# Kernel tuning notes

Measured on AMD Instinct MI355X. Metric: run time of the kernel, lower is better.

The kernel has to match this reference:

```python
import jax, jax.numpy as jnp
import numpy as np

B, T, D = 32, 1024, 256
TOP_K = 2
EPS_ADJ = 1e-6
LN_EPS = 1e-5


def setup_inputs() -> dict:
    key = jax.random.key(0)
    ks = jax.random.split(key, 10)
    inp = {
        'x': jax.random.normal(ks[0], (B, T, D), dtype=jnp.float32),
        'mask': jnp.ones((B, T), dtype=jnp.int32),
    }
    # two GCN layers: linear W [D_out, D_in] (torch layout), bias, LayerNorm gamma/beta
    for li in range(2):
        inp[f'W{li}'] = jax.random.normal(ks[1 + 4 * li], (D, D), dtype=jnp.float32) * (1.0 / np.sqrt(D))
        inp[f'b{li}'] = jax.random.normal(ks[2 + 4 * li], (D,), dtype=jnp.float32) * 0.02
        inp[f'g{li}'] = jnp.ones((D,), dtype=jnp.float32)
        inp[f'be{li}'] = jnp.zeros((D,), dtype=jnp.float32)
    return inp


def _layer_norm(x, gamma, beta):
    mu = jnp.mean(x, axis=-1, keepdims=True)
    var = jnp.mean(jnp.square(x - mu), axis=-1, keepdims=True)
    return (x - mu) * jax.lax.rsqrt(var + LN_EPS) * gamma + beta


def _cos_sim(x, maskf):
    x_norm = x / jnp.clip(jnp.linalg.norm(x, axis=-1, keepdims=True), 1e-12)
    sim = jnp.einsum('bid,bjd->bij', x_norm, x_norm)
    return sim * (maskf[:, :, None] * maskf[:, None, :])


def _build_adj(sim, maskf):
    b, t, _ = sim.shape
    eye = jnp.eye(t, dtype=sim.dtype)
    # temporal chain edges + self loops
    base_adj = eye + jnp.eye(t, k=1, dtype=sim.dtype) + jnp.eye(t, k=-1, dtype=sim.dtype)
    # top-k over similarity with diagonal suppressed
    corel = jnp.where(eye[None] == 1, -1.0, sim)
    _, topk_inds = jax.lax.top_k(corel, TOP_K)  # [B, T, K]
    bi = jnp.arange(b)[:, None, None]
    ii = jnp.arange(t)[None, :, None]
    ext = jnp.zeros_like(sim).at[bi, ii, topk_inds].set(1.0)
    ext = jnp.maximum(ext, jnp.swapaxes(ext, 1, 2))
    ext = ext * (maskf[:, :, None] * maskf[:, None, :])
    adj = jnp.clip(base_adj[None] + ext, 0.0, 1.0) * sim + eye[None]
    row_sum = jnp.sum(adj, axis=-1, keepdims=True) + EPS_ADJ
    col_sum = jnp.sum(adj, axis=1, keepdims=True) + EPS_ADJ
    adj = adj / jnp.sqrt(row_sum * col_sum)
    return adj * (maskf[:, :, None] * maskf[:, None, :])


def reference(x, mask, W0, b0, g0, be0, W1, b1, g1, be1):
    maskf = mask.astype(x.dtype)
    sim = _cos_sim(x, maskf)
    adj = _build_adj(sim, maskf)
    params = [(W0, b0, g0, be0), (W1, b1, g1, be1)]
    h = x
    for (W, bb, g, be) in params:
        h = jnp.einsum('bij,bjd->bid', adj, h)
        h = jnp.einsum('bid,od->bio', h, W) + bb
        h = jax.nn.elu(h)
        h = _layer_norm(h, g, be)
        # dropout: identity in eval mode
    return h
```

## Files before the change

kernel.cpp:

```cpp
#include <hip/hip_runtime.h>
#include <math.h>

#define NB 32
#define NT 1024
#define ND 256
#define NROWS (NB*NT)
#define MAXE 64

typedef __attribute__((ext_vector_type(8))) short bf16x8;
typedef __attribute__((ext_vector_type(4))) float f32x4;
typedef unsigned short ushort_t;
typedef unsigned long long u64;

__device__ inline ushort_t f2bf_rn(float f){
  unsigned u = __float_as_uint(f);
  unsigned r = u + 0x7fffu + ((u >> 16) & 1u);
  return (ushort_t)(r >> 16);
}
__device__ inline float bf2f(ushort_t h){
  return __uint_as_float(((unsigned)h) << 16);
}
__device__ inline void ceswap(u64 &a, u64 &b){
  u64 mx = a > b ? a : b;
  u64 mn = a > b ? b : a;
  a = mx; b = mn;
}
__device__ inline u64 umax64(u64 a, u64 b){ return a > b ? a : b; }

__device__ inline void gld16(const ushort_t* g, ushort_t* l){
  __builtin_amdgcn_global_load_lds(
      (const __attribute__((address_space(1))) unsigned int*)(g),
      (__attribute__((address_space(3))) unsigned int*)(l),
      16, 0, 0);
}

__global__ __launch_bounds__(256) void k_norm(const float* __restrict__ x,
                                              float* __restrict__ xn,
                                              ushort_t* __restrict__ xh,
                                              ushort_t* __restrict__ xl){
  int row = blockIdx.x;
  int t = threadIdx.x;
  size_t base = (size_t)row*ND;
  float v = x[base + t];
  float ss = v*v;
  #pragma unroll
  for (int off=32; off; off>>=1) ss += __shfl_xor(ss, off);
  __shared__ float sred[4];
  if ((t & 63) == 0) sred[t>>6] = ss;
  __syncthreads();
  float tot = sred[0] + sred[1] + sred[2] + sred[3];
  float nrm = fmaxf(sqrtf(tot), 1e-12f);
  float res = v / nrm;
  xn[base + t] = res;
  ushort_t hb = f2bf_rn(res);
  float lres = res - bf2f(hb);
  xh[base + t] = hb;
  xl[base + t] = f2bf_rn(lres);
}

__global__ __launch_bounds__(256) void k_wsplit(const float* __restrict__ W0,
                                                const float* __restrict__ W1,
                                                ushort_t* __restrict__ Wh0, ushort_t* __restrict__ Wl0,
                                                ushort_t* __restrict__ Wh1, ushort_t* __restrict__ Wl1){
  int idx = blockIdx.x*256 + threadIdx.x;
  float w0 = W0[idx]; ushort_t h0 = f2bf_rn(w0);
  Wh0[idx] = h0; Wl0[idx] = f2bf_rn(w0 - bf2f(h0));
  float w1 = W1[idx]; ushort_t h1 = f2bf_rn(w1);
  Wh1[idx] = h1; Wl1[idx] = f2bf_rn(w1 - bf2f(h1));
}

__global__ __launch_bounds__(256) void k_sim(const ushort_t* __restrict__ xh,
                                             const ushort_t* __restrict__ xl,
                                             ushort_t* __restrict__ S,
                                             int bat0){
  __shared__ __align__(16) ushort_t Ahs[128*64];
  __shared__ __align__(16) ushort_t Als[128*64];
  __shared__ __align__(16) ushort_t Bhs[128*64];
  __shared__ __align__(16) ushort_t Bls[128*64];

  int blk0 = blockIdx.x;
  int blk = (blk0 & 7)*128 + (blk0 >> 3);

  int b_local = blk >> 6;
  int b = bat0 + b_local;
  int tt = blk & 63;
  int ti = tt >> 3, tj = tt & 7;
  int i0 = ti*128, j0 = tj*128;

  int t = threadIdx.x;
  int lane = t & 63, wave = t >> 6;
  int wy = wave >> 1, wx = wave & 1;
  int c = lane & 15, q = lane >> 4;
  int lrow = lane >> 3;
  int sc   = (lane & 7) ^ lrow;

  f32x4 acc[4][4];
  #pragma unroll
  for (int bi=0;bi<4;bi++)
    #pragma unroll
    for (int bj=0;bj<4;bj++) acc[bi][bj] = {0.f,0.f,0.f,0.f};

  size_t rowbA = (size_t)(b*NT + i0);
  size_t rowbB = (size_t)(b*NT + j0);
  const ushort_t* Agh = xh + rowbA*ND;
  const ushort_t* Agl = xl + rowbA*ND;
  const ushort_t* Bgh = xh + rowbB*ND;
  const ushort_t* Bgl = xl + rowbB*ND;

  for (int kc=0; kc<4; kc++){
    __syncthreads();
    int koff = kc*64;
    #pragma unroll
    for (int inst=0; inst<4; inst++){
      int r0 = wave*32 + inst*8;
      size_t go = (size_t)(r0 + lrow)*ND + koff + sc*8;
      gld16(Agh + go, &Ahs[r0*64]);
      gld16(Agl + go, &Als[r0*64]);
      gld16(Bgh + go, &Bhs[r0*64]);
      gld16(Bgl + go, &Bls[r0*64]);
    }
    __syncthreads();

    #pragma unroll
    for (int ks=0; ks<2; ks++){
      bf16x8 ah[4], al[4], bh[4], bl[4];
      int slot = (ks*4 + q) ^ (c & 7);
      #pragma unroll
      for (int bi=0;bi<4;bi++){
        int row = wy*64 + bi*16 + c;
        ah[bi] = *(const bf16x8*)&Ahs[row*64 + slot*8];
        al[bi] = *(const bf16x8*)&Als[row*64 + slot*8];
      }
      #pragma unroll
      for (int bj=0;bj<4;bj++){
        int row = wx*64 + bj*16 + c;
        bh[bj] = *(const bf16x8*)&Bhs[row*64 + slot*8];
        bl[bj] = *(const bf16x8*)&Bls[row*64 + slot*8];
      }
      #pragma unroll
      for (int bi=0;bi<4;bi++)
        #pragma unroll
        for (int bj=0;bj<4;bj++){
          acc[bi][bj] = __builtin_amdgcn_mfma_f32_16x16x32_bf16(ah[bi], bh[bj], acc[bi][bj], 0, 0, 0);
          acc[bi][bj] = __builtin_amdgcn_mfma_f32_16x16x32_bf16(al[bi], bh[bj], acc[bi][bj], 0, 0, 0);
          acc[bi][bj] = __builtin_amdgcn_mfma_f32_16x16x32_bf16(ah[bi], bl[bj], acc[bi][bj], 0, 0, 0);
        }
    }
  }

  size_t srow0 = (size_t)b_local*NT + i0 + wy*64;
  int col0 = j0 + wx*64;
  #pragma unroll
  for (int bi=0;bi<4;bi++){
    #pragma unroll
    for (int reg=0;reg<4;reg++){
      ushort_t* dst = S + (srow0 + bi*16 + q*4 + reg)*NT + col0;
      #pragma unroll
      for (int bj=0;bj<4;bj++)
        dst[bj*16 + c] = f2bf_rn(acc[bi][bj][reg]);
    }
  }
}

__global__ __launch_bounds__(256) void k_top8(const ushort_t* __restrict__ S,
                                              int4* __restrict__ cand4,
                                              int rowbase){
  int row = blockIdx.x*4 + (threadIdx.x >> 6);
  int lane = threadIdx.x & 63;
  int i = row & 1023;
  const ushort_t* Sr = S + (size_t)row*NT;
  u64 e0 = 0, e1 = 0;
  #pragma unroll
  for (int seg=0; seg<4; seg++){
    int col = seg*256 + lane*4;
    u64 v4 = *(const u64*)&Sr[col];
    #pragma unroll
    for (int m=0;m<4;m++){
      unsigned u = (unsigned)((v4 >> (16*m)) & 0xffffu) << 16;
      unsigned key = u ^ ((unsigned)((int)u >> 31) | 0x80000000u);
      int j = col + m;
      u64 e = ((u64)key << 32) | (unsigned)j;
      if (j == i) e = 0;
      u64 mn = e0 > e ? e : e0;
      e0 = e0 > e ? e0 : e;
      e1 = e1 > mn ? e1 : mn;
    }
  }
  u64 L0 = e0, L1 = e1, L2 = 0, L3 = 0;
  #pragma unroll
  for (int st=1; st<64; st<<=1){
    u64 R0 = __shfl_xor(L0, st), R1 = __shfl_xor(L1, st);
    u64 R2 = __shfl_xor(L2, st), R3 = __shfl_xor(L3, st);
    u64 m0 = umax64(L0, R3), m1 = umax64(L1, R2);
    u64 m2 = umax64(L2, R1), m3 = umax64(L3, R0);
    ceswap(m0, m2); ceswap(m1, m3); ceswap(m0, m1); ceswap(m2, m3);
    L0 = m0; L1 = m1; L2 = m2; L3 = m3;
  }
  if (lane == 0)
    cand4[rowbase + row] = make_int4((int)(unsigned)L0, (int)(unsigned)L1,
                                     (int)(unsigned)L2, (int)(unsigned)L3);
}

__global__ __launch_bounds__(64) void k_refine4(const float* __restrict__ xn,
                                                const int4* __restrict__ cand4,
                                                int2* __restrict__ top2){
  int row = blockIdx.x; int b = row >> 10, i = row & 1023;
  int l = threadIdx.x;
  const float* Xb = xn + (size_t)b*NT*ND;
  float4 xi = *(const float4*)&Xb[(size_t)i*ND + l*4];
  int4 cd = cand4[row];
  int cands[4] = {cd.x, cd.y, cd.z, cd.w};
  double bv1=-1e30, bv2=-1e30; int bi1=0x7fffffff, bi2=0x7fffffff;
  #pragma unroll
  for (int cq=0;cq<4;cq++){
    int j = cands[cq];
    float4 xj = *(const float4*)&Xb[(size_t)j*ND + l*4];
    double p = (double)xi.x*xj.x + (double)xi.y*xj.y
             + (double)xi.z*xj.z + (double)xi.w*xj.w;
    #pragma unroll
    for (int off=32; off; off>>=1) p += __shfl_xor(p, off);
    if (p > bv1 || (p == bv1 && j < bi1)) { bv2=bv1; bi2=bi1; bv1=p; bi1=j; }
    else if (p > bv2 || (p == bv2 && j < bi2)) { bv2=p; bi2=j; }
  }
  if (l == 0) top2[row] = make_int2(bi1, bi2);
}

__global__ __launch_bounds__(256) void k_scatter(const int2* __restrict__ top2,
                                                 unsigned* __restrict__ ext){
  int row = blockIdx.x*256 + threadIdx.x;
  int b = row >> 10, i = row & 1023;
  int2 tp = top2[row];
  unsigned* eb = ext + (size_t)b*NT*32;
  int j1 = tp.x, j2 = tp.y;
  atomicOr(&eb[(size_t)i*32 + (j1>>5)], 1u << (j1&31));
  atomicOr(&eb[(size_t)j1*32 + (i>>5)], 1u << (i&31));
  atomicOr(&eb[(size_t)i*32 + (j2>>5)], 1u << (j2&31));
  atomicOr(&eb[(size_t)j2*32 + (i>>5)], 1u << (i&31));
}

__global__ __launch_bounds__(64) void k_edges(const float* __restrict__ xn,
                                              const unsigned* __restrict__ ext,
                                              int* __restrict__ eidx,
                                              float* __restrict__ eval_,
                                              float* __restrict__ rs,
                                              int* __restrict__ ecnt){
  int row = blockIdx.x; int b = row >> 10, i = row & 1023;
  int l = threadIdx.x;
  const float* Xb = xn + (size_t)b*NT*ND;
  float4 xi = *(const float4*)&Xb[(size_t)i*ND + l*4];
  unsigned word = 0;
  if (l < 32){
    word = ext[((size_t)b*NT + i)*32 + l];
    int js[3] = {i-1, i, i+1};
    #pragma unroll
    for (int qd=0;qd<3;qd++){
      int j = js[qd];
      if (j >= 0 && j < NT && (j>>5) == l) word |= (1u << (j&31));
    }
  }
  float rsum = 0.f; int cnt = 0;
  for (int w=0; w<32; w++){
    unsigned bits = __shfl(word, w);
    while (bits){
      int bit = __ffs(bits) - 1;
      bits &= bits - 1;
      int j = w*32 + bit;
      float4 xj = *(const float4*)&Xb[(size_t)j*ND + l*4];
      float p = xi.x*xj.x + xi.y*xj.y + xi.z*xj.z + xi.w*xj.w;
      #pragma unroll
      for (int off=32; off; off>>=1) p += __shfl_xor(p, off);
      float v = p + ((j==i) ? 1.0f : 0.0f);
      if (l == 0 && cnt < MAXE){
        eidx[(size_t)row*MAXE + cnt] = j;
        eval_[(size_t)row*MAXE + cnt] = v;
      }
      rsum += v; cnt++;
    }
  }
  if (l == 0){ rs[row] = rsum + 1e-6f; ecnt[row] = (cnt < MAXE) ? cnt : MAXE; }
}

__global__ __launch_bounds__(256) void k_wnorm(const int* __restrict__ eidx,
                                               const float* __restrict__ eval_,
                                               const float* __restrict__ rs,
                                               const int* __restrict__ ecnt,
                                               float* __restrict__ wn){
  int row = blockIdx.x*4 + (threadIdx.x >> 6);
  int lane = threadIdx.x & 63;
  int b = row >> 10;
  int n = ecnt[row];
  float rsi = rs[row];
  if (lane < n){
    int j = eidx[(size_t)row*MAXE + lane];
    float v = eval_[(size_t)row*MAXE + lane];
    wn[(size_t)row*MAXE + lane] = v / sqrtf(rsi * rs[b*NT + j]);
  }
}

__global__ __launch_bounds__(256) void k_spmm(const float* __restrict__ hin,
                                              const int* __restrict__ eidx,
                                              const float* __restrict__ wn,
                                              const int* __restrict__ ecnt,
                                              float* __restrict__ hout){
  int row = blockIdx.x*4 + (threadIdx.x >> 6);
  int lane = threadIdx.x & 63;
  int b = row >> 10;
  const float* Hb = hin + (size_t)b*NT*ND;
  int n = ecnt[row];
  const int* ei = eidx + (size_t)row*MAXE;
  const float* we = wn + (size_t)row*MAXE;
  float4 acc = {0.f,0.f,0.f,0.f};
  int e = 0;
  for (; e+2 <= n; e += 2){
    int j0 = ei[e],   j1 = ei[e+1];
    float w0 = we[e], w1 = we[e+1];
    float4 v0 = *(const float4*)&Hb[(size_t)j0*ND + lane*4];
    float4 v1 = *(const float4*)&Hb[(size_t)j1*ND + lane*4];
    acc.x += w0*v0.x; acc.y += w0*v0.y; acc.z += w0*v0.z; acc.w += w0*v0.w;
    acc.x += w1*v1.x; acc.y += w1*v1.y; acc.z += w1*v1.z; acc.w += w1*v1.w;
  }
  if (e < n){
    int j0 = ei[e]; float w0 = we[e];
    float4 v0 = *(const float4*)&Hb[(size_t)j0*ND + lane*4];
    acc.x += w0*v0.x; acc.y += w0*v0.y; acc.z += w0*v0.z; acc.w += w0*v0.w;
  }
  *(float4*)&hout[(size_t)row*ND + lane*4] = acc;
}

__global__ __launch_bounds__(256) void k_dense2(const float* __restrict__ hs,
                                                const ushort_t* __restrict__ Wh,
                                                const ushort_t* __restrict__ Wl,
                                                const float* __restrict__ bias,
                                                const float* __restrict__ gam,
                                                const float* __restrict__ bet,
                                                float* __restrict__ out){
  __shared__ __align__(16) ushort_t Ah[64*72];
  __shared__ __align__(16) ushort_t Al[64*72];
  __shared__ float sums[64*4];
  __shared__ float sqs[64*4];
  __shared__ float muA[64];
  __shared__ float rsA[64];

  int t = threadIdx.x;
  int lane = t & 63, wave = t >> 6;
  int c = lane & 15, q = lane >> 4;
  size_t row0 = (size_t)blockIdx.x * 64;

  f32x4 acc[4][4];
  #pragma unroll
  for (int bi=0;bi<4;bi++)
    #pragma unroll
    for (int bj=0;bj<4;bj++) acc[bi][bj] = {0.f,0.f,0.f,0.f};

  for (int kc=0; kc<4; kc++){
    __syncthreads();
    {
      int r = t >> 2, csg = (t & 3) * 16;
      const float* src = &hs[(row0 + r)*ND + kc*64 + csg];
      float4 f0 = *(const float4*)&src[0];
      float4 f1 = *(const float4*)&src[4];
      float4 f2 = *(const float4*)&src[8];
      float4 f3 = *(const float4*)&src[12];
      float fa[16] = {f0.x,f0.y,f0.z,f0.w, f1.x,f1.y,f1.z,f1.w,
                      f2.x,f2.y,f2.z,f2.w, f3.x,f3.y,f3.z,f3.w};
      bf16x8 h8[2], l8[2];
      #pragma unroll
      for (int g=0; g<2; g++){
        #pragma unroll
        for (int m=0; m<8; m++){
          float f = fa[g*8 + m];
          ushort_t hb = f2bf_rn(f);
          h8[g][m] = (short)hb;
          l8[g][m] = (short)f2bf_rn(f - bf2f(hb));
        }
      }
      *(bf16x8*)&Ah[r*72 + csg]     = h8[0];
      *(bf16x8*)&Ah[r*72 + csg + 8] = h8[1];
      *(bf16x8*)&Al[r*72 + csg]     = l8[0];
      *(bf16x8*)&Al[r*72 + csg + 8] = l8[1];
    }
    __syncthreads();
    #pragma unroll
    for (int ks=0; ks<2; ks++){
      bf16x8 ah[4], al[4], wh[4], wl[4];
      #pragma unroll
      for (int bi=0;bi<4;bi++){
        ah[bi] = *(const bf16x8*)&Ah[(bi*16+c)*72 + ks*32 + q*8];
        al[bi] = *(const bf16x8*)&Al[(bi*16+c)*72 + ks*32 + q*8];
      }
      #pragma unroll
      for (int bj=0;bj<4;bj++){
        size_t wo = (size_t)(wave*64 + bj*16 + c)*ND + kc*64 + ks*32 + q*8;
        wh[bj] = *(const bf16x8*)&Wh[wo];
        wl[bj] = *(const bf16x8*)&Wl[wo];
      }
      #pragma unroll
      for (int bi=0;bi<4;bi++)
        #pragma unroll
        for (int bj=0;bj<4;bj++){
          acc[bi][bj] = __builtin_amdgcn_mfma_f32_16x16x32_bf16(ah[bi], wh[bj], acc[bi][bj], 0, 0, 0);
          acc[bi][bj] = __builtin_amdgcn_mfma_f32_16x16x32_bf16(al[bi], wh[bj], acc[bi][bj], 0, 0, 0);
          acc[bi][bj] = __builtin_amdgcn_mfma_f32_16x16x32_bf16(ah[bi], wl[bj], acc[bi][bj], 0, 0, 0);
        }
    }
  }

  float bv[4], gv[4], tv[4];
  #pragma unroll
  for (int bj=0;bj<4;bj++){
    int col = wave*64 + bj*16 + c;
    bv[bj] = bias[col]; gv[bj] = gam[col]; tv[bj] = bet[col];
  }
  #pragma unroll
  for (int bi=0;bi<4;bi++)
    #pragma unroll
    for (int bj=0;bj<4;bj++)
      #pragma unroll
      for (int reg=0;reg<4;reg++){
        float v = acc[bi][bj][reg] + bv[bj];
        acc[bi][bj][reg] = (v > 0.f) ? v : expm1f(v);
      }

  #pragma unroll
  for (int bi=0;bi<4;bi++)
    #pragma unroll
    for (int reg=0;reg<4;reg++){
      float s = acc[bi][0][reg] + acc[bi][1][reg] + acc[bi][2][reg] + acc[bi][3][reg];
      #pragma unroll
      for (int st=1; st<16; st<<=1) s += __shfl_xor(s, st);
      if (c == 0) sums[(bi*16 + q*4 + reg)*4 + wave] = s;
    }
  __syncthreads();
  if (t < 64){
    float s = sums[t*4] + sums[t*4+1] + sums[t*4+2] + sums[t*4+3];
    muA[t] = s * (1.0f/ND);
  }
  __syncthreads();
  #pragma unroll
  for (int bi=0;bi<4;bi++)
    #pragma unroll
    for (int reg=0;reg<4;reg++){
      float mu = muA[bi*16 + q*4 + reg];
      float ss = 0.f;
      #pragma unroll
      for (int bj=0;bj<4;bj++){ float d = acc[bi][bj][reg] - mu; ss += d*d; }
      #pragma unroll
      for (int st=1; st<16; st<<=1) ss += __shfl_xor(ss, st);
      if (c == 0) sqs[(bi*16 + q*4 + reg)*4 + wave] = ss;
    }
  __syncthreads();
  if (t < 64){
    float ss = sqs[t*4] + sqs[t*4+1] + sqs[t*4+2] + sqs[t*4+3];
    rsA[t] = rsqrtf(ss * (1.0f/ND) + 1e-5f);
  }
  __syncthreads();
  #pragma unroll
  for (int bi=0;bi<4;bi++)
    #pragma unroll
    for (int reg=0;reg<4;reg++){
      int row = bi*16 + q*4 + reg;
      float mu = muA[row], rst = rsA[row];
      #pragma unroll
      for (int bj=0;bj<4;bj++){
        float val = (acc[bi][bj][reg] - mu) * rst * gv[bj] + tv[bj];
        out[(row0 + row)*ND + wave*64 + bj*16 + c] = val;
      }
    }
}

extern "C" void kernel_launch(void* const* d_in, const int* in_sizes, int n_in,
                              void* d_out, int out_size, void* d_ws, size_t ws_size,
                              hipStream_t stream) {
  (void)in_sizes; (void)n_in; (void)out_size; (void)ws_size;
  const float* x   = (const float*)d_in[0];
  const float* W0  = (const float*)d_in[2];
  const float* b0  = (const float*)d_in[3];
  const float* g0  = (const float*)d_in[4];
  const float* be0 = (const float*)d_in[5];
  const float* W1  = (const float*)d_in[6];
  const float* b1  = (const float*)d_in[7];
  const float* g1  = (const float*)d_in[8];
  const float* be1 = (const float*)d_in[9];
  float* out = (float*)d_out;

  char* wsb = (char*)d_ws;
  float* xn = (float*)wsb;
  ushort_t* xh = (ushort_t*)(wsb + (size_t)32*1024*1024);
  ushort_t* xl = (ushort_t*)(wsb + (size_t)48*1024*1024);
  float* hsbuf = (float*)xh;
  char* zc = wsb + (size_t)64*1024*1024;
  ushort_t* S = (ushort_t*)zc;
  unsigned* ext   = (unsigned*)zc;
  int*      eidx  = (int*)(zc + (size_t)4*1024*1024);
  float*    eval_ = (float*)(zc + (size_t)12*1024*1024);
  float*    rs    = (float*)(zc + (size_t)20*1024*1024);
  int*      ecnt  = (int*)(zc + (size_t)21*1024*1024);
  float*    wn    = (float*)(zc + (size_t)22*1024*1024);
  char* zd = wsb + (size_t)98*1024*1024;
  int4* cand4 = (int4*)zd;
  int2* top2  = (int2*)(zd + (size_t)512*1024);
  ushort_t* Wh0 = (ushort_t*)(zd + (size_t)1024*1024);
  ushort_t* Wl0 = Wh0 + 65536;
  ushort_t* Wh1 = Wl0 + 65536;
  ushort_t* Wl1 = Wh1 + 65536;

  k_wsplit<<<256, 256, 0, stream>>>(W0, W1, Wh0, Wl0, Wh1, Wl1);
  k_norm<<<NROWS, 256, 0, stream>>>(x, xn, xh, xl);
  for (int h=0; h<2; h++){
    int bat0 = h*16;
    k_sim<<<1024, 256, 0, stream>>>(xh, xl, S, bat0);
    k_top8<<<4096, 256, 0, stream>>>(S, cand4, bat0*NT);
  }
  k_refine4<<<NROWS, 64, 0, stream>>>(xn, cand4, top2);
  hipMemsetAsync(ext, 0, (size_t)NROWS*32*4, stream);
  k_scatter<<<NROWS/256, 256, 0, stream>>>(top2, ext);
  k_edges<<<NROWS, 64, 0, stream>>>(xn, ext, eidx, eval_, rs, ecnt);
  k_wnorm<<<NROWS/4, 256, 0, stream>>>(eidx, eval_, rs, ecnt, wn);
  k_spmm<<<NROWS/4, 256, 0, stream>>>(x, eidx, wn, ecnt, hsbuf);
  k_dense2<<<NROWS/64, 256, 0, stream>>>(hsbuf, Wh0, Wl0, b0, g0, be0, out);
  k_spmm<<<NROWS/4, 256, 0, stream>>>(out, eidx, wn, ecnt, hsbuf);
  k_dense2<<<NROWS/64, 256, 0, stream>>>(hsbuf, Wh1, Wl1, b1, g1, be1, out);
}
```

Baseline: 389.7 us.

## Emit bf16 hi/lo split from SpMM and enlarge dense tile with async LDS loads

The SpMM kernel now writes its output directly as bf16 high/low halves, so the dense kernel no longer reads fp32 and converts it. The dense kernel moves to 128-row tiles with 512 threads arranged as 2x4 waves. It loads A tiles with direct global-to-LDS 16-byte loads (gld16) into an XOR-swizzled layout in place of padded rows. Together these cut conversion work, halve the reloads of W per row, and reduce LDS bank conflicts, at the cost of more registers and LDS per block and a dependence on gld16 being defined in the unseen part of the file.

Result: no change. 387.6 us (-0.5%).

```diff
diff --git a/kernel.cpp b/kernel.cpp
--- a/kernel.cpp
+++ b/kernel.cpp
@@ -301,7 +301,8 @@
                                               const int* __restrict__ eidx,
                                               const float* __restrict__ wn,
                                               const int* __restrict__ ecnt,
-                                              float* __restrict__ hout){
+                                              ushort_t* __restrict__ Hh,
+                                              ushort_t* __restrict__ Hl){
   int row = blockIdx.x*4 + (threadIdx.x >> 6);
   int lane = threadIdx.x & 63;
   int b = row >> 10;
@@ -324,27 +325,44 @@
     float4 v0 = *(const float4*)&Hb[(size_t)j0*ND + lane*4];
     acc.x += w0*v0.x; acc.y += w0*v0.y; acc.z += w0*v0.z; acc.w += w0*v0.w;
   }
-  *(float4*)&hout[(size_t)row*ND + lane*4] = acc;
-}
-
-__global__ __launch_bounds__(256) void k_dense2(const float* __restrict__ hs,
+  float av[4] = {acc.x, acc.y, acc.z, acc.w};
+  u64 ph = 0, pl = 0;
+  #pragma unroll
+  for (int m=0;m<4;m++){
+    ushort_t hb = f2bf_rn(av[m]);
+    ushort_t lb = f2bf_rn(av[m] - bf2f(hb));
+    ph |= (u64)hb << (16*m);
+    pl |= (u64)lb << (16*m);
+  }
+  *(u64*)&Hh[(size_t)row*ND + lane*4] = ph;
+  *(u64*)&Hl[(size_t)row*ND + lane*4] = pl;
+}
+
+__global__ __launch_bounds__(512) void k_dense2(const ushort_t* __restrict__ Hh,
+                                                const ushort_t* __restrict__ Hl,
                                                 const ushort_t* __restrict__ Wh,
                                                 const ushort_t* __restrict__ Wl,
                                                 const float* __restrict__ bias,
                                                 const float* __restrict__ gam,
                                                 const float* __restrict__ bet,
                                                 float* __restrict__ out){
-  __shared__ __align__(16) ushort_t Ah[64*72];
-  __shared__ __align__(16) ushort_t Al[64*72];
-  __shared__ float sums[64*4];
-  __shared__ float sqs[64*4];
-  __shared__ float muA[64];
-  __shared__ float rsA[64];
+  __shared__ __align__(16) ushort_t Ahs[128*64];
+  __shared__ __align__(16) ushort_t Als[128*64];
+  __shared__ float sums[128*4];
+  __shared__ float sqs[128*4];
+  __shared__ float muA[128];
+  __shared__ float rsA[128];
 
   int t = threadIdx.x;
   int lane = t & 63, wave = t >> 6;
+  int wy = wave >> 2, wx = wave & 3;
   int c = lane & 15, q = lane >> 4;
-  size_t row0 = (size_t)blockIdx.x * 64;
+  int lrow = lane >> 3;
+  int sc   = (lane & 7) ^ lrow;
+  size_t row0 = (size_t)blockIdx.x * 128;
+
+  const ushort_t* Hhb = Hh + row0*ND;
+  const ushort_t* Hlb = Hl + row0*ND;
 
   f32x4 acc[4][4];
   #pragma unroll
@@ -354,45 +372,31 @@
 
   for (int kc=0; kc<4; kc++){
     __syncthreads();
-    {
-      int r = t >> 2, csg = (t & 3) * 16;
-      const float* src = &hs[(row0 + r)*ND + kc*64 + csg];
-      float4 f0 = *(const float4*)&src[0];
-      float4 f1 = *(const float4*)&src[4];
-      float4 f2 = *(const float4*)&src[8];
-      float4 f3 = *(const float4*)&src[12];
-      float fa[16] = {f0.x,f0.y,f0.z,f0.w, f1.x,f1.y,f1.z,f1.w,
-                      f2.x,f2.y,f2.z,f2.w, f3.x,f3.y,f3.z,f3.w};
-      bf16x8 h8[2], l8[2];
-      #pragma unroll
-      for (int g=0; g<2; g++){
-        #pragma unroll
-        for (int m=0; m<8; m++){
-          float f = fa[g*8 + m];
-          ushort_t hb = f2bf_rn(f);
-          h8[g][m] = (short)hb;
-          l8[g][m] = (short)f2bf_rn(f - bf2f(hb));
-        }
-      }
-      *(bf16x8*)&Ah[r*72 + csg]     = h8[0];
-      *(bf16x8*)&Ah[r*72 + csg + 8] = h8[1];
-      *(bf16x8*)&Al[r*72 + csg]     = l8[0];
-      *(bf16x8*)&Al[r*72 + csg + 8] = l8[1];
+    int koff = kc*64;
+    #pragma unroll
+    for (int inst=0; inst<2; inst++){
+      int r0 = wave*16 + inst*8;
+      size_t go = (size_t)(r0 + lrow)*ND + koff + sc*8;
+      gld16(Hhb + go, &Ahs[r0*64]);
+      gld16(Hlb + go, &Als[r0*64]);
     }
     __syncthreads();
+
     #pragma unroll
     for (int ks=0; ks<2; ks++){
       bf16x8 ah[4], al[4], wh[4], wl[4];
       #pragma unroll
-      for (int bi=0;bi<4;bi++){
-        ah[bi] = *(const bf16x8*)&Ah[(bi*16+c)*72 + ks*32 + q*8];
-        al[bi] = *(const bf16x8*)&Al[(bi*16+c)*72 + ks*32 + q*8];
-      }
-      #pragma unroll
       for (int bj=0;bj<4;bj++){
-        size_t wo = (size_t)(wave*64 + bj*16 + c)*ND + kc*64 + ks*32 + q*8;
+        size_t wo = (size_t)(wx*64 + bj*16 + c)*ND + koff + ks*32 + q*8;
         wh[bj] = *(const bf16x8*)&Wh[wo];
         wl[bj] = *(const bf16x8*)&Wl[wo];
+      }
+      int slot = (ks*4 + q) ^ (c & 7);
+      #pragma unroll
+      for (int bi=0;bi<4;bi++){
+        int row = wy*64 + bi*16 + c;
+        ah[bi] = *(const bf16x8*)&Ahs[row*64 + slot*8];
+        al[bi] = *(const bf16x8*)&Als[row*64 + slot*8];
       }
       #pragma unroll
       for (int bi=0;bi<4;bi++)
@@ -408,7 +412,7 @@
   float bv[4], gv[4], tv[4];
   #pragma unroll
   for (int bj=0;bj<4;bj++){
-    int col = wave*64 + bj*16 + c;
+    int col = wx*64 + bj*16 + c;
     bv[bj] = bias[col]; gv[bj] = gam[col]; tv[bj] = bet[col];
   }
   #pragma unroll
@@ -428,10 +432,10 @@
       float s = acc[bi][0][reg] + acc[bi][1][reg] + acc[bi][2][reg] + acc[bi][3][reg];
       #pragma unroll
       for (int st=1; st<16; st<<=1) s += __shfl_xor(s, st);
-      if (c == 0) sums[(bi*16 + q*4 + reg)*4 + wave] = s;
+      if (c == 0) sums[(wy*64 + bi*16 + q*4 + reg)*4 + wx] = s;
     }
   __syncthreads();
-  if (t < 64){
+  if (t < 128){
     float s = sums[t*4] + sums[t*4+1] + sums[t*4+2] + sums[t*4+3];
     muA[t] = s * (1.0f/ND);
   }
@@ -440,16 +444,16 @@
   for (int bi=0;bi<4;bi++)
     #pragma unroll
     for (int reg=0;reg<4;reg++){
-      float mu = muA[bi*16 + q*4 + reg];
+      float mu = muA[wy*64 + bi*16 + q*4 + reg];
       float ss = 0.f;
       #pragma unroll
       for (int bj=0;bj<4;bj++){ float d = acc[bi][bj][reg] - mu; ss += d*d; }
       #pragma unroll
       for (int st=1; st<16; st<<=1) ss += __shfl_xor(ss, st);
-      if (c == 0) sqs[(bi*16 + q*4 + reg)*4 + wave] = ss;
+      if (c == 0) sqs[(wy*64 + bi*16 + q*4 + reg)*4 + wx] = ss;
     }
   __syncthreads();
-  if (t < 64){
+  if (t < 128){
     float ss = sqs[t*4] + sqs[t*4+1] + sqs[t*4+2] + sqs[t*4+3];
     rsA[t] = rsqrtf(ss * (1.0f/ND) + 1e-5f);
   }
@@ -458,12 +462,12 @@
   for (int bi=0;bi<4;bi++)
     #pragma unroll
     for (int reg=0;reg<4;reg++){
-      int row = bi*16 + q*4 + reg;
+      int row = wy*64 + bi*16 + q*4 + reg;
       float mu = muA[row], rst = rsA[row];
       #pragma unroll
       for (int bj=0;bj<4;bj++){
         float val = (acc[bi][bj][reg] - mu) * rst * gv[bj] + tv[bj];
-        out[(row0 + row)*ND + wave*64 + bj*16 + c] = val;
+        out[(row0 + row)*ND + wx*64 + bj*16 + c] = val;
       }
     }
 }
@@ -487,7 +491,8 @@
   float* xn = (float*)wsb;
   ushort_t* xh = (ushort_t*)(wsb + (size_t)32*1024*1024);
   ushort_t* xl = (ushort_t*)(wsb + (size_t)48*1024*1024);
-  float* hsbuf = (float*)xh;
+  ushort_t* hh = xh;
+  ushort_t* hl = xl;
   char* zc = wsb + (size_t)64*1024*1024;
   ushort_t* S = (ushort_t*)zc;
   unsigned* ext   = (unsigned*)zc;
@@ -516,8 +521,8 @@
   k_scatter<<<NROWS/256, 256, 0, stream>>>(top2, ext);
   k_edges<<<NROWS, 64, 0, stream>>>(xn, ext, eidx, eval_, rs, ecnt);
   k_wnorm<<<NROWS/4, 256, 0, stream>>>(eidx, eval_, rs, ecnt, wn);
-  k_spmm<<<NROWS/4, 256, 0, stream>>>(x, eidx, wn, ecnt, hsbuf);
-  k_dense2<<<NROWS/64, 256, 0, stream>>>(hsbuf, Wh0, Wl0, b0, g0, be0, out);
-  k_spmm<<<NROWS/4, 256, 0, stream>>>(out, eidx, wn, ecnt, hsbuf);
-  k_dense2<<<NROWS/64, 256, 0, stream>>>(hsbuf, Wh1, Wl1, b1, g1, be1, out);
-}
+  k_spmm<<<NROWS/4, 256, 0, stream>>>(x, eidx, wn, ecnt, hh, hl);
+  k_dense2<<<NROWS/128, 512, 0, stream>>>(hh, hl, Wh0, Wl0, b0, g0, be0, out);
+  k_spmm<<<NROWS/4, 256, 0, stream>>>(out, eidx, wn, ecnt, hh, hl);
+  k_dense2<<<NROWS/128, 512, 0, stream>>>(hh, hl, Wh1, Wl1, b1, g1, be1, out);
+}
```
